# Performance work log

Hardware: AMD Instinct MI355X
Metric: run time of the kernel (lower is better)

## Reference

```python
import jax, jax.numpy as jnp
import numpy as np

B, N, C = 2, 2048, 1024
H, D = 16, 64  # n_q_heads, head_dim
EPS = 1e-6


def setup_inputs() -> dict:
    key = jax.random.key(0)
    ks = jax.random.split(key, 6)
    x = jax.random.normal(ks[0], (B, N, C), dtype=jnp.float32)
    context = jax.random.normal(ks[1], (B, N, C), dtype=jnp.float32)
    # realistic RoPE tables, rotary_dim = head_dim (non-interleaved GLM-style)
    inv_freq = 1.0 / (10000.0 ** (np.arange(0, D, 2, dtype=np.float32) / D))
    ang = np.arange(N, dtype=np.float32)[:, None] * inv_freq[None, :]  # [N, D/2]
    ang = np.concatenate([ang, ang], axis=-1)  # [N, D]
    cos = jnp.broadcast_to(jnp.cos(ang)[None], (B, N, D)).astype(jnp.float32)
    sin = jnp.broadcast_to(jnp.sin(ang)[None], (B, N, D)).astype(jnp.float32)
    s = 1.0 / np.sqrt(C)
    Wq = jax.random.normal(ks[2], (2 * C, C), dtype=jnp.float32) * s
    Wkv = jax.random.normal(ks[3], (2 * C, C), dtype=jnp.float32) * s
    Wo = jax.random.normal(ks[4], (C, C), dtype=jnp.float32) * s
    bo = jnp.zeros((C,), dtype=jnp.float32)
    q_norm_w = jnp.ones((D,), dtype=jnp.float32)
    k_norm_w = jnp.ones((D,), dtype=jnp.float32)
    return {"x": x, "context": context, "cos": cos, "sin": sin,
            "Wq": Wq, "Wkv": Wkv, "Wo": Wo, "bo": bo,
            "q_norm_w": q_norm_w, "k_norm_w": k_norm_w}


def _zm_rmsnorm(t, w):
    # zero-mean RMSNorm over last (head_dim) axis: LayerNorm without bias
    t = t - jnp.mean(t, axis=-1, keepdims=True)
    var = jnp.mean(t * t, axis=-1, keepdims=True)
    return t * jax.lax.rsqrt(var + EPS) * w


def _rotate_half(t):
    t1, t2 = jnp.split(t, 2, axis=-1)
    return jnp.concatenate([-t2, t1], axis=-1)


def reference(x, context, cos, sin, Wq, Wkv, Wo, bo, q_norm_w, k_norm_w):
    b, n1, c = x.shape
    n2 = context.shape[1]
    # fused q+gate projection: [b, n1, 2*C] -> [b, n1, H, 2D], per-head chunk
    qg = (x @ Wq.T).reshape(b, n1, H, 2 * D)
    q = qg[..., :D]                      # [b, n1, H, D]
    gate = qg[..., D:].reshape(b, n1, H * D)  # [b, n1, C]
    q = _zm_rmsnorm(q, q_norm_w).transpose(0, 2, 1, 3)  # [b, H, n1, D]
    # fused k+v projection: [b, n2, 2*C] -> [b, n2, H, 2D]
    kv = (context @ Wkv.T).reshape(b, n2, H, 2 * D)
    k = _zm_rmsnorm(kv[..., :D], k_norm_w).transpose(0, 2, 1, 3)  # [b, H, n2, D]
    v = kv[..., D:].transpose(0, 2, 1, 3)                         # [b, H, n2, D]
    # RoPE (full head_dim rotary)
    cos_b = cos[:, None]  # [b, 1, n, D]
    sin_b = sin[:, None]
    q = q * cos_b + _rotate_half(q) * sin_b
    k = k * cos_b + _rotate_half(k) * sin_b
    # SDPA (non-causal cross attention)
    scale = D ** -0.5
    scores = jnp.einsum('bhqd,bhkd->bhqk', q, k) * scale
    attn = jax.nn.softmax(scores, axis=-1)
    attn_out = jnp.einsum('bhqk,bhkd->bhqd', attn, v)
    attn_out = attn_out.transpose(0, 2, 1, 3).reshape(b, n1, H * D)  # [b, n1, C]
    # gated output combine + out projection
    attn_out = attn_out * jax.nn.sigmoid(gate)
    return attn_out @ Wo.T + bo
```

## Files before the change

kernel.cpp:

```cpp
#include <hip/hip_runtime.h>
#include <cstdint>
#include <cstddef>


#define B_ 2
#define N_ 2048
#define C_ 1024
#define H_ 16
#define D_ 64
#define K_ 1024
#define PK_ 2048
#define EPS_ 1e-6f
#define LOG2E_ 1.44269504088896f
#define SMAX_ 12.0f

typedef __bf16 b16x8 __attribute__((ext_vector_type(8)));
typedef float f32x4 __attribute__((ext_vector_type(4)));

__device__ __forceinline__ unsigned short f2bf(float f) {
  union { float f; unsigned u; } a; a.f = f;
  unsigned r = a.u + 0x7FFFu + ((a.u >> 16) & 1u);
  return (unsigned short)(r >> 16);
}
__device__ __forceinline__ float bf2f(unsigned short u) {
  union { unsigned u; float f; } a; a.u = ((unsigned)u) << 16; return a.f;
}

__device__ __forceinline__ void cast_one(const float* __restrict__ src,
                                         unsigned short* __restrict__ dst, int e) {
  float4 v = *(const float4*)(src + e);
  *(ushort4*)(dst + e) = make_ushort4(f2bf(v.x), f2bf(v.y), f2bf(v.z), f2bf(v.w));
}

__device__ __forceinline__ void pack_one(const float* __restrict__ src,
                                         unsigned short* __restrict__ dst, int e) {
  float4 v = *(const float4*)(src + e);
  const int r = e >> 10, k = e & 1023;
  unsigned short* p = dst + ((size_t)r << 11) + ((k >> 5) << 6) + (k & 31);
  const unsigned short h0 = f2bf(v.x), h1 = f2bf(v.y), h2 = f2bf(v.z), h3 = f2bf(v.w);
  *(ushort4*)p = make_ushort4(h0, h1, h2, h3);
  *(ushort4*)(p + 32) = make_ushort4(f2bf(v.x - bf2f(h0)), f2bf(v.y - bf2f(h1)),
                                     f2bf(v.z - bf2f(h2)), f2bf(v.w - bf2f(h3)));
}

__global__ __launch_bounds__(256) void pack_all(
    const float* __restrict__ x, const float* __restrict__ Wq,
    const float* __restrict__ ctx, const float* __restrict__ Wkv,
    const float* __restrict__ Wo,
    unsigned short* __restrict__ xb, unsigned short* __restrict__ wqb,
    unsigned short* __restrict__ cb, unsigned short* __restrict__ wkvb,
    unsigned short* __restrict__ wop)
{
  const int e = (blockIdx.x * 256 + threadIdx.x) << 2;
  if (e < 4194304)       cast_one(x,   xb,  e);
  else if (e < 6291456)  cast_one(Wq,  wqb, e - 4194304);
  else if (e < 10485760) cast_one(ctx, cb,  e - 6291456);
  else if (e < 12582912) cast_one(Wkv, wkvb, e - 10485760);
  else                   pack_one(Wo,  wop, e - 12582912);
}

__global__ __launch_bounds__(512, 2) void gemm_qkv(
    const unsigned short* __restrict__ xb, const unsigned short* __restrict__ wqb,
    const unsigned short* __restrict__ cb, const unsigned short* __restrict__ wkvb,
    const float* __restrict__ cosb, const float* __restrict__ sinb,
    const float* __restrict__ qnw, const float* __restrict__ knw,
    unsigned short* __restrict__ Qbo, unsigned short* __restrict__ Kbo,
    unsigned short* __restrict__ gate, unsigned short* __restrict__ vt, float qscale)
{
  __shared__ __align__(16) unsigned short As[2][256 * 64];
  __shared__ __align__(16) unsigned short Bs[2][256 * 64];
  const int tid = threadIdx.x, lane = tid & 63, wave = tid >> 6;

  const int id = blockIdx.x;
  const int swz = (id & 7) * 32 + (id >> 3);
  const bool isQ = swz < 128;
  const int local = swz & 127;
  const int bm = (local >> 3) << 8, bn = (local & 7) << 8;
  const int wm = (wave >> 2) << 7, wn = (wave & 3) << 6;

  const unsigned short* Ap = isQ ? xb : cb;
  const unsigned short* Bp = isQ ? wqb : wkvb;

  const int srow = lane >> 3;
  const int sslot = (lane & 7) ^ srow;
  const size_t rbytes = (size_t)K_ * 2;
  const char* aSrc = (const char*)Ap + (size_t)(bm + srow) * rbytes + (sslot << 4);
  const char* bSrc = (const char*)Bp + (size_t)(bn + srow) * rbytes + (sslot << 4);

  f32x4 acc[8][4];
  #pragma unroll
  for (int i = 0; i < 8; ++i)
    #pragma unroll
    for (int j = 0; j < 4; ++j) acc[i][j] = (f32x4){0.f, 0.f, 0.f, 0.f};

  const int fr = lane & 15, fs = lane >> 4;

  #define QSTAGE(buf, kt)                                                          \
    {                                                                              \
      const size_t ko = (size_t)(kt) << 7;                                         \
      _Pragma("unroll")                                                            \
      for (int i = 0; i < 4; ++i) {                                                \
        const int g = (wave << 2) + i;                                             \
        __builtin_amdgcn_global_load_lds(                                          \
            (const __attribute__((address_space(1))) void*)(aSrc + (size_t)(g << 3) * rbytes + ko), \
            (__attribute__((address_space(3))) void*)((char*)As[buf] + (g << 10)), \
            16, 0, 0);                                                             \
        __builtin_amdgcn_global_load_lds(                                          \
            (const __attribute__((address_space(1))) void*)(bSrc + (size_t)(g << 3) * rbytes + ko), \
            (__attribute__((address_space(3))) void*)((char*)Bs[buf] + (g << 10)), \
            16, 0, 0);                                                             \
      }                                                                            \
    }

  QSTAGE(0, 0);
  int cur = 0;
  for (int kt = 0; kt < 16; ++kt) {
    __syncthreads();
    if (kt + 1 < 16) QSTAGE(cur ^ 1, kt + 1);

    const char* Abuf = (const char*)As[cur];
    const char* Bbuf = (const char*)Bs[cur];
    __builtin_amdgcn_s_setprio(1);
    #pragma unroll
    for (int kk = 0; kk < 2; ++kk) {
      b16x8 a[8], b[4];
      #pragma unroll
      for (int mi = 0; mi < 8; ++mi) {
        const int ar = wm + (mi << 4) + fr;
        a[mi] = *(const b16x8*)(Abuf + (ar << 7) + ((((kk << 2) + fs) ^ (ar & 7)) << 4));
      }
      #pragma unroll
      for (int ni = 0; ni < 4; ++ni) {
        const int br = wn + (ni << 4) + fr;
        b[ni] = *(const b16x8*)(Bbuf + (br << 7) + ((((kk << 2) + fs) ^ (br & 7)) << 4));
      }
      #pragma unroll
      for (int mi = 0; mi < 8; ++mi)
        #pragma unroll
        for (int ni = 0; ni < 4; ++ni)
          acc[mi][ni] = __builtin_amdgcn_mfma_f32_16x16x32_bf16(a[mi], b[ni], acc[mi][ni], 0, 0, 0);
    }
    __builtin_amdgcn_s_setprio(0);
    cur ^= 1;
  }
  #undef QSTAGE

  const int g = lane >> 4;
  const int h = (bn >> 7) + (wn >> 7);
  const bool normHalf = ((wn >> 6) & 1) == 0;
  if (normHalf) {
    const float* nw = isQ ? qnw : knw;
    const float oscale = isQ ? qscale : 1.0f;
    unsigned short* nOut = isQ ? Qbo : Kbo;
    float wv[4];
    #pragma unroll
    for (int ni = 0; ni < 4; ++ni) wv[ni] = nw[(ni << 4) + fr];
    #pragma unroll
    for (int mi = 0; mi < 8; ++mi) {
      #pragma unroll
      for (int r = 0; r < 4; ++r) {
        const int t = bm + wm + (mi << 4) + (g << 2) + r;
        float v0 = acc[mi][0][r], v1 = acc[mi][1][r];
        float v2 = acc[mi][2][r], v3 = acc[mi][3][r];
        float s = (v0 + v1) + (v2 + v3);
        #pragma unroll
        for (int off = 1; off < 16; off <<= 1) s += __shfl_xor(s, off);
        const float mean = s * (1.f / 64.f);
        v0 -= mean; v1 -= mean; v2 -= mean; v3 -= mean;
        float s2 = (v0*v0 + v1*v1) + (v2*v2 + v3*v3);
        #pragma unroll
        for (int off = 1; off < 16; off <<= 1) s2 += __shfl_xor(s2, off);
        const float rq = rsqrtf(s2 * (1.f / 64.f) + EPS_);
        const float x0 = v0 * rq * wv[0], x1 = v1 * rq * wv[1];
        const float x2 = v2 * rq * wv[2], x3 = v3 * rq * wv[3];
        const float* cr = cosb + (size_t)t * 64;
        const float* sr = sinb + (size_t)t * 64;
        const float o0 = x0 * cr[fr]    - x2 * sr[fr];
        const float o1 = x1 * cr[16+fr] - x3 * sr[16+fr];
        const float o2 = x2 * cr[32+fr] + x0 * sr[32+fr];
        const float o3 = x3 * cr[48+fr] + x1 * sr[48+fr];
        unsigned short* dp = nOut + (((size_t)((t >> 11) * H_ + h)) * N_ + (t & 2047)) * 64;
        dp[fr]      = f2bf(o0 * oscale);
        dp[16 + fr] = f2bf(o1 * oscale);
        dp[32 + fr] = f2bf(o2 * oscale);
        dp[48 + fr] = f2bf(o3 * oscale);
      }
    }
  } else if (isQ) {
    #pragma unroll
    for (int mi = 0; mi < 8; ++mi)
      #pragma unroll
      for (int r = 0; r < 4; ++r) {
        const int t = bm + wm + (mi << 4) + (g << 2) + r;
        unsigned short* gp = gate + (size_t)t * C_ + h * 64;
        #pragma unroll
        for (int ni = 0; ni < 4; ++ni) gp[(ni << 4) + fr] = f2bf(acc[mi][ni][r]);
      }
  } else {
    #pragma unroll
    for (int mi = 0; mi < 8; ++mi) {
      const int t0 = bm + wm + (mi << 4) + (g << 2);
      const int bb = t0 >> 11, n0 = t0 & 2047;
      #pragma unroll
      for (int ni = 0; ni < 4; ++ni) {
        const int dv = (ni << 4) + fr;
        ushort4 pk = make_ushort4(f2bf(acc[mi][ni][0]), f2bf(acc[mi][ni][1]),
                                  f2bf(acc[mi][ni][2]), f2bf(acc[mi][ni][3]));
        *(ushort4*)(vt + ((size_t)(bb * H_ + h) * 64 + dv) * N_ + n0) = pk;
      }
    }
  }
}

__global__ __launch_bounds__(256) void gemm_nt_hilo(
    const unsigned short* __restrict__ Ap, const unsigned short* __restrict__ Bp,
    float* __restrict__ Cm, int M, int N, const float* __restrict__ bias)
{
  __shared__ __align__(16) unsigned short As[128 * 64];
  __shared__ __align__(16) unsigned short Bs[64 * 64];
  const int tid = threadIdx.x, lane = tid & 63, wave = tid >> 6;

  const int nwg = gridDim.x, id = blockIdx.x;
  const int swz = (id & 7) * (nwg >> 3) + (id >> 3);
  const int nbn = N >> 6;
  const int bm = (swz / nbn) << 7, bn = (swz % nbn) << 6;
  const int wm = (wave >> 1) << 6, wn = (wave & 1) << 5;

  const int srow = lane >> 3;
  const int sslot = (lane & 7) ^ srow;
  const size_t rbytes = (size_t)K_ * 4;
  const char* aSrc = (const char*)Ap + (size_t)(bm + srow) * rbytes + (sslot << 4);
  const char* bSrc = (const char*)Bp + (size_t)(bn + srow) * rbytes + (sslot << 4);

  f32x4 acc[4][2];
  #pragma unroll
  for (int i = 0; i < 4; ++i)
    #pragma unroll
    for (int j = 0; j < 2; ++j) acc[i][j] = (f32x4){0.f, 0.f, 0.f, 0.f};

  const int fr = lane & 15, fs = lane >> 4;
  const int hoff = (fs ^ (fr & 7)) << 4;

  for (int ks = 0; ks < K_ / 32; ++ks) {
    const size_t ko = (size_t)ks << 7;
    #pragma unroll
    for (int i = 0; i < 4; ++i) {
      const int ga = (wave << 2) + i;
      __builtin_amdgcn_global_load_lds(
          (const __attribute__((address_space(1))) void*)(aSrc + (size_t)(ga << 3) * rbytes + ko),
          (__attribute__((address_space(3))) void*)((char*)As + (ga << 10)), 16, 0, 0);
    }
    #pragma unroll
    for (int i = 0; i < 2; ++i) {
      const int gb = (wave << 1) + i;
      __builtin_amdgcn_global_load_lds(
          (const __attribute__((address_space(1))) void*)(bSrc + (size_t)(gb << 3) * rbytes + ko),
          (__attribute__((address_space(3))) void*)((char*)Bs + (gb << 10)), 16, 0, 0);
    }
    __syncthreads();

    b16x8 ah[4], al[4], bh[2], bl[2];
    #pragma unroll
    for (int t = 0; t < 4; ++t) {
      const char* pa = (const char*)As + ((wm + (t << 4) + fr) << 7);
      ah[t] = *(const b16x8*)(pa + hoff);
      al[t] = *(const b16x8*)(pa + (hoff ^ 64));
    }
    #pragma unroll
    for (int t = 0; t < 2; ++t) {
      const char* pb = (const char*)Bs + ((wn + (t << 4) + fr) << 7);
      bh[t] = *(const b16x8*)(pb + hoff);
      bl[t] = *(const b16x8*)(pb + (hoff ^ 64));
    }
    #pragma unroll
    for (int mi = 0; mi < 4; ++mi)
      #pragma unroll
      for (int ni = 0; ni < 2; ++ni) {
        acc[mi][ni] = __builtin_amdgcn_mfma_f32_16x16x32_bf16(ah[mi], bh[ni], acc[mi][ni], 0, 0, 0);
        acc[mi][ni] = __builtin_amdgcn_mfma_f32_16x16x32_bf16(al[mi], bh[ni], acc[mi][ni], 0, 0, 0);
        acc[mi][ni] = __builtin_amdgcn_mfma_f32_16x16x32_bf16(ah[mi], bl[ni], acc[mi][ni], 0, 0, 0);
      }
    __syncthreads();
  }

  const int rbase = (lane >> 4) << 2;
  #pragma unroll
  for (int mi = 0; mi < 4; ++mi)
    #pragma unroll
    for (int ni = 0; ni < 2; ++ni) {
      const int n = bn + wn + (ni << 4) + fr;
      const float badd = bias ? bias[n] : 0.f;
      #pragma unroll
      for (int r = 0; r < 4; ++r) {
        const int m = bm + wm + (mi << 4) + rbase + r;
        Cm[(size_t)m * N + n] = acc[mi][ni][r] + badd;
      }
    }
}

__global__ __launch_bounds__(256) void flash_bf16(
    const unsigned short* __restrict__ Qb, const unsigned short* __restrict__ Kb,
    const unsigned short* __restrict__ Vt, const unsigned short* __restrict__ gateb,
    unsigned short* __restrict__ gp)
{
  const int id = blockIdx.x;
  const int swzb = (id & 7) * 64 + (id >> 3);
  const int q0 = (swzb & 15) * 128;
  const int h = (swzb >> 4) & 15;
  const int b = swzb >> 8;
  const int tid = threadIdx.x, lane = tid & 63, wave = tid >> 6;
  __shared__ __align__(16) unsigned short Ks[2][64 * 64];
  __shared__ __align__(16) unsigned short Vss[2][64 * 64];
  __shared__ __align__(16) __bf16 Ps[4][2][16][72];
  const int bh = b * H_ + h;
  const int g = lane >> 4, fr = lane & 15;

  b16x8 qA0, qA1, qB0, qB1;
  {
    const unsigned short* QrowA = Qb + ((size_t)bh * N_ + q0 + wave*32 + fr) * D_;
    qA0 = *(const b16x8*)(QrowA + (g << 3));
    qA1 = *(const b16x8*)(QrowA + 32 + (g << 3));
    qB0 = *(const b16x8*)(QrowA + 16 * D_ + (g << 3));
    qB1 = *(const b16x8*)(QrowA + 16 * D_ + 32 + (g << 3));
  }

  f32x4 oA[4], oB[4];
  #pragma unroll
  for (int r = 0; r < 4; ++r) {
    oA[r] = (f32x4){0.f, 0.f, 0.f, 0.f};
    oB[r] = (f32x4){0.f, 0.f, 0.f, 0.f};
  }
  float lA = 0.f, lB = 0.f;

  const unsigned short* Kbh  = Kb + (size_t)bh * N_ * D_;
  const unsigned short* Vtbh = Vt + (size_t)bh * D_ * N_;
  const int swzK = ((lane & 7) ^ (lane >> 3)) << 4;
  __bf16* PwA = &Ps[wave][0][0][0] + fr * 72;
  __bf16* PwB = &Ps[wave][1][0][0] + fr * 72;

  #define STAGE(buf, j0)                                                          \
    {                                                                             \
      _Pragma("unroll")                                                           \
      for (int i = 0; i < 2; ++i) {                                               \
        const int gg = wave * 2 + i;                                              \
        const char* ksrc = (const char*)(Kbh + (size_t)((j0) + gg * 8) * D_) +    \
                           (lane >> 3) * 128 + swzK;                              \
        __builtin_amdgcn_global_load_lds(                                         \
            (const __attribute__((address_space(1))) void*)ksrc,                  \
            (__attribute__((address_space(3))) void*)((char*)Ks[buf] + gg * 1024),\
            16, 0, 0);                                                            \
        const int dv = gg * 8 + (lane >> 3);                                      \
        const char* vsrc = (const char*)(Vtbh + (size_t)dv * N_ + (j0)) + swzK;   \
        __builtin_amdgcn_global_load_lds(                                         \
            (const __attribute__((address_space(1))) void*)vsrc,                  \
            (__attribute__((address_space(3))) void*)((char*)Vss[buf] + gg * 1024),\
            16, 0, 0);                                                            \
      }                                                                           \
    }

  STAGE(0, 0);
  int cur = 0;
  for (int j0 = 0; j0 < N_; j0 += 64) {
    __syncthreads();
    if (j0 + 64 < N_) STAGE(cur ^ 1, j0 + 64);

    const unsigned short* Kbuf = Ks[cur];
    const unsigned short* Vbuf = Vss[cur];
    const int cb0 = g << 4;
    __builtin_amdgcn_s_setprio(1);
    #pragma unroll
    for (int t = 0; t < 4; ++t) {
      const int krow = t * 16 + fr;
      const char* kbp = (const char*)Kbuf + krow * 128;
      const int f = (krow & 7) << 4;
      b16x8 kf0 = *(const b16x8*)(kbp + (cb0 ^ f));
      b16x8 kf1 = *(const b16x8*)(kbp + ((64 + cb0) ^ f));
      f32x4 sA = __builtin_amdgcn_mfma_f32_16x16x32_bf16(kf0, qA0, (f32x4){0.f,0.f,0.f,0.f}, 0, 0, 0);
      sA = __builtin_amdgcn_mfma_f32_16x16x32_bf16(kf1, qA1, sA, 0, 0, 0);
      f32x4 sB = __builtin_amdgcn_mfma_f32_16x16x32_bf16(kf0, qB0, (f32x4){0.f,0.f,0.f,0.f}, 0, 0, 0);
      sB = __builtin_amdgcn_mfma_f32_16x16x32_bf16(kf1, qB1, sB, 0, 0, 0);
      union { __bf16 hb[4]; ushort4 u4; } pkA, pkB;
      #pragma unroll
      for (int r = 0; r < 4; ++r) {
        const float pA = __builtin_amdgcn_exp2f(sA[r] - SMAX_);
        lA += pA;
        pkA.hb[r] = (__bf16)pA;
        const float pB = __builtin_amdgcn_exp2f(sB[r] - SMAX_);
        lB += pB;
        pkB.hb[r] = (__bf16)pB;
      }
      *(ushort4*)(PwA + t * 16 + (g << 2)) = pkA.u4;
      *(ushort4*)(PwB + t * 16 + (g << 2)) = pkB.u4;
    }
    __builtin_amdgcn_s_setprio(0);

    b16x8 pfA[2], pfB[2];
    #pragma unroll
    for (int c = 0; c < 2; ++c) {
      pfA[c] = *(const b16x8*)(PwA + c * 32 + (g << 3));
      pfB[c] = *(const b16x8*)(PwB + c * 32 + (g << 3));
    }

    __builtin_amdgcn_s_setprio(1);
    #pragma unroll
    for (int dt = 0; dt < 4; ++dt) {
      const int vrow = dt * 16 + fr;
      const char* vbp = (const char*)Vbuf + vrow * 128;
      const int fv = (vrow & 7) << 4;
      #pragma unroll
      for (int c = 0; c < 2; ++c) {
        b16x8 vf = *(const b16x8*)(vbp + ((c * 64 + cb0) ^ fv));
        oA[dt] = __builtin_amdgcn_mfma_f32_16x16x32_bf16(pfA[c], vf, oA[dt], 0, 0, 0);
        oB[dt] = __builtin_amdgcn_mfma_f32_16x16x32_bf16(pfB[c], vf, oB[dt], 0, 0, 0);
      }
    }
    __builtin_amdgcn_s_setprio(0);
    cur ^= 1;
  }
  #undef STAGE

  lA += __shfl_xor(lA, 16); lA += __shfl_xor(lA, 32);
  lB += __shfl_xor(lB, 16); lB += __shfl_xor(lB, 32);

  #pragma unroll
  for (int r = 0; r < 4; ++r) {
    const float lqA = __shfl(lA, (g << 2) + r);
    const float lqB = __shfl(lB, (g << 2) + r);
    #pragma unroll
    for (int set = 0; set < 2; ++set) {
      const float inv = 1.f / (set ? lqB : lqA);
      const int q = q0 + wave * 32 + set * 16 + (g << 2) + r;
      const size_t qa = (size_t)(b * N_ + q);
      #pragma unroll
      for (int dt = 0; dt < 4; ++dt) {
        const int d = (dt << 4) + fr;
        const float o = (set ? oB[dt][r] : oA[dt][r]) * inv;
        const float gate = bf2f(gateb[qa * C_ + h * 64 + d]);
        const float sg = 1.f / (1.f + __expf(-gate));
        const float val = o * sg;
        const int k = h * 64 + d;
        unsigned short* p = gp + qa * PK_ + ((k >> 5) << 6) + (k & 31);
        const unsigned short hi = f2bf(val);
        p[0]  = hi;
        p[32] = f2bf(val - bf2f(hi));
      }
    }
  }
}

extern "C" void kernel_launch(void* const* d_in, const int* in_sizes, int n_in,
                              void* d_out, int out_size, void* d_ws, size_t ws_size,
                              hipStream_t stream) {
  const float* x    = (const float*)d_in[0];
  const float* ctx  = (const float*)d_in[1];
  const float* cosb = (const float*)d_in[2];
  const float* sinb = (const float*)d_in[3];
  const float* Wq   = (const float*)d_in[4];
  const float* Wkv  = (const float*)d_in[5];
  const float* Wo   = (const float*)d_in[6];
  const float* bo   = (const float*)d_in[7];
  const float* qnw  = (const float*)d_in[8];
  const float* knw  = (const float*)d_in[9];
  float* out = (float*)d_out;

  char* ws = (char*)d_ws;
  unsigned short* Qb   = (unsigned short*)(ws);
  unsigned short* Kb   = (unsigned short*)(ws + (size_t)8388608);
  unsigned short* Vt   = (unsigned short*)(ws + (size_t)16777216);
  unsigned short* gate = (unsigned short*)(ws + (size_t)25165824);
  unsigned short* gpk  = (unsigned short*)(ws + (size_t)41943040);
  unsigned short* xb   = (unsigned short*)(ws + (size_t)58720256);
  unsigned short* cb   = (unsigned short*)(ws + (size_t)67108864);
  unsigned short* wqb  = (unsigned short*)(ws + (size_t)75497472);
  unsigned short* wkvb = (unsigned short*)(ws + (size_t)79691776);
  unsigned short* wop  = (unsigned short*)(ws + (size_t)83886080);

  pack_all<<<dim3(13312), dim3(256), 0, stream>>>(x, Wq, ctx, Wkv, Wo, xb, wqb, cb, wkvb, wop);
  gemm_qkv<<<dim3(256), dim3(512), 0, stream>>>(xb, wqb, cb, wkvb, cosb, sinb, qnw, knw,
                                                Qb, Kb, gate, Vt, 0.125f * LOG2E_);
  flash_bf16<<<dim3(512), dim3(256), 0, stream>>>(Qb, Kb, Vt, gate, gpk);
  gemm_nt_hilo<<<dim3(512), dim3(256), 0, stream>>>(gpk, wop, out, 4096, 1024, bo);
}
```

Before: 150.4 us.

## Load K fragments directly into registers with double-buffered prefetch

The K tile no longer goes through LDS via global_load_lds. Each wave reads its K MFMA fragments straight from global memory into registers, one tile ahead, ping-ponging between two register sets while V keeps its LDS double buffer. This drops the K LDS traffic and its footprint but increases register pressure. Every wave also redundantly loads the same K rows from global/L2 instead of sharing one staged copy.

```diff
diff --git a/kernel.cpp b/kernel.cpp
--- a/kernel.cpp
+++ b/kernel.cpp
@@ -309,7 +309,6 @@
   const int h = (swzb >> 4) & 15;
   const int b = swzb >> 8;
   const int tid = threadIdx.x, lane = tid & 63, wave = tid >> 6;
-  __shared__ __align__(16) unsigned short Ks[2][64 * 64];
   __shared__ __align__(16) unsigned short Vss[2][64 * 64];
   __shared__ __align__(16) __bf16 Ps[4][2][16][72];
   const int bh = b * H_ + h;
@@ -338,17 +337,11 @@
   __bf16* PwA = &Ps[wave][0][0][0] + fr * 72;
   __bf16* PwB = &Ps[wave][1][0][0] + fr * 72;
 
-  #define STAGE(buf, j0)                                                          \
+  #define STAGE_V(buf, j0)                                                        \
     {                                                                             \
       _Pragma("unroll")                                                           \
       for (int i = 0; i < 2; ++i) {                                               \
         const int gg = wave * 2 + i;                                              \
-        const char* ksrc = (const char*)(Kbh + (size_t)((j0) + gg * 8) * D_) +    \
-                           (lane >> 3) * 128 + swzK;                              \
-        __builtin_amdgcn_global_load_lds(                                         \
-            (const __attribute__((address_space(1))) void*)ksrc,                  \
-            (__attribute__((address_space(3))) void*)((char*)Ks[buf] + gg * 1024),\
-            16, 0, 0);                                                            \
         const int dv = gg * 8 + (lane >> 3);                                      \
         const char* vsrc = (const char*)(Vtbh + (size_t)dv * N_ + (j0)) + swzK;   \
         __builtin_amdgcn_global_load_lds(                                         \
@@ -358,66 +351,74 @@
       }                                                                           \
     }
 
-  STAGE(0, 0);
-  int cur = 0;
-  for (int j0 = 0; j0 < N_; j0 += 64) {
-    __syncthreads();
-    if (j0 + 64 < N_) STAGE(cur ^ 1, j0 + 64);
-
-    const unsigned short* Kbuf = Ks[cur];
-    const unsigned short* Vbuf = Vss[cur];
-    const int cb0 = g << 4;
-    __builtin_amdgcn_s_setprio(1);
-    #pragma unroll
-    for (int t = 0; t < 4; ++t) {
-      const int krow = t * 16 + fr;
-      const char* kbp = (const char*)Kbuf + krow * 128;
-      const int f = (krow & 7) << 4;
-      b16x8 kf0 = *(const b16x8*)(kbp + (cb0 ^ f));
-      b16x8 kf1 = *(const b16x8*)(kbp + ((64 + cb0) ^ f));
-      f32x4 sA = __builtin_amdgcn_mfma_f32_16x16x32_bf16(kf0, qA0, (f32x4){0.f,0.f,0.f,0.f}, 0, 0, 0);
-      sA = __builtin_amdgcn_mfma_f32_16x16x32_bf16(kf1, qA1, sA, 0, 0, 0);
-      f32x4 sB = __builtin_amdgcn_mfma_f32_16x16x32_bf16(kf0, qB0, (f32x4){0.f,0.f,0.f,0.f}, 0, 0, 0);
-      sB = __builtin_amdgcn_mfma_f32_16x16x32_bf16(kf1, qB1, sB, 0, 0, 0);
-      union { __bf16 hb[4]; ushort4 u4; } pkA, pkB;
-      #pragma unroll
-      for (int r = 0; r < 4; ++r) {
-        const float pA = __builtin_amdgcn_exp2f(sA[r] - SMAX_);
-        lA += pA;
-        pkA.hb[r] = (__bf16)pA;
-        const float pB = __builtin_amdgcn_exp2f(sB[r] - SMAX_);
-        lB += pB;
-        pkB.hb[r] = (__bf16)pB;
-      }
-      *(ushort4*)(PwA + t * 16 + (g << 2)) = pkA.u4;
-      *(ushort4*)(PwB + t * 16 + (g << 2)) = pkB.u4;
-    }
-    __builtin_amdgcn_s_setprio(0);
-
-    b16x8 pfA[2], pfB[2];
-    #pragma unroll
-    for (int c = 0; c < 2; ++c) {
-      pfA[c] = *(const b16x8*)(PwA + c * 32 + (g << 3));
-      pfB[c] = *(const b16x8*)(PwB + c * 32 + (g << 3));
-    }
-
-    __builtin_amdgcn_s_setprio(1);
-    #pragma unroll
-    for (int dt = 0; dt < 4; ++dt) {
-      const int vrow = dt * 16 + fr;
-      const char* vbp = (const char*)Vbuf + vrow * 128;
-      const int fv = (vrow & 7) << 4;
-      #pragma unroll
-      for (int c = 0; c < 2; ++c) {
-        b16x8 vf = *(const b16x8*)(vbp + ((c * 64 + cb0) ^ fv));
-        oA[dt] = __builtin_amdgcn_mfma_f32_16x16x32_bf16(pfA[c], vf, oA[dt], 0, 0, 0);
-        oB[dt] = __builtin_amdgcn_mfma_f32_16x16x32_bf16(pfB[c], vf, oB[dt], 0, 0, 0);
-      }
-    }
-    __builtin_amdgcn_s_setprio(0);
-    cur ^= 1;
-  }
-  #undef STAGE
+  #define LOADK(K0, K1, j0)                                                       \
+    {                                                                             \
+      _Pragma("unroll")                                                           \
+      for (int t = 0; t < 4; ++t) {                                               \
+        const unsigned short* kr = Kbh + (size_t)((j0) + t * 16 + fr) * D_ + (g << 3); \
+        K0[t] = *(const b16x8*)(kr);                                              \
+        K1[t] = *(const b16x8*)(kr + 32);                                         \
+      }                                                                           \
+    }
+
+  #define TILE(KC0, KC1, KN0, KN1, buf, j0, jn)                                   \
+    {                                                                             \
+      __syncthreads();                             \
+      if ((jn) < N_) { STAGE_V((buf) ^ 1, jn); LOADK(KN0, KN1, jn); }             \
+      const int cb0 = g << 4;                                                     \
+      __builtin_amdgcn_s_setprio(1);                                              \
+      _Pragma("unroll")                                                           \
+      for (int t = 0; t < 4; ++t) {                                               \
+        f32x4 sA = __builtin_amdgcn_mfma_f32_16x16x32_bf16(KC0[t], qA0, (f32x4){0.f,0.f,0.f,0.f}, 0, 0, 0); \
+        sA = __builtin_amdgcn_mfma_f32_16x16x32_bf16(KC1[t], qA1, sA, 0, 0, 0);   \
+        f32x4 sB = __builtin_amdgcn_mfma_f32_16x16x32_bf16(KC0[t], qB0, (f32x4){0.f,0.f,0.f,0.f}, 0, 0, 0); \
+        sB = __builtin_amdgcn_mfma_f32_16x16x32_bf16(KC1[t], qB1, sB, 0, 0, 0);   \
+        union { __bf16 hb[4]; ushort4 u4; } pkA, pkB;                             \
+        _Pragma("unroll")                                                         \
+        for (int r = 0; r < 4; ++r) {                                             \
+          const float pA = __builtin_amdgcn_exp2f(sA[r] - SMAX_);                 \
+          lA += pA;                                                               \
+          pkA.hb[r] = (__bf16)pA;                                                 \
+          const float pB = __builtin_amdgcn_exp2f(sB[r] - SMAX_);                 \
+          lB += pB;                                                               \
+          pkB.hb[r] = (__bf16)pB;                                                 \
+        }                                                                         \
+        *(ushort4*)(PwA + t * 16 + (g << 2)) = pkA.u4;                            \
+        *(ushort4*)(PwB + t * 16 + (g << 2)) = pkB.u4;                            \
+      }                                                                           \
+      __builtin_amdgcn_s_setprio(0);                                              \
+      b16x8 pfA[2], pfB[2];                                                       \
+      _Pragma("unroll")                                                           \
+      for (int c = 0; c < 2; ++c) {                                               \
+        pfA[c] = *(const b16x8*)(PwA + c * 32 + (g << 3));                        \
+        pfB[c] = *(const b16x8*)(PwB + c * 32 + (g << 3));                        \
+      }                                                                           \
+      __builtin_amdgcn_s_setprio(1);                                              \
+      _Pragma("unroll")                                                           \
+      for (int dt = 0; dt < 4; ++dt) {                                            \
+        const int vrow = dt * 16 + fr;                                            \
+        const char* vbp = (const char*)Vss[buf] + vrow * 128;                     \
+        const int fv = (vrow & 7) << 4;                                           \
+        _Pragma("unroll")                                                         \
+        for (int c = 0; c < 2; ++c) {                                             \
+          b16x8 vf = *(const b16x8*)(vbp + ((c * 64 + cb0) ^ fv));                \
+          oA[dt] = __builtin_amdgcn_mfma_f32_16x16x32_bf16(pfA[c], vf, oA[dt], 0, 0, 0); \
+          oB[dt] = __builtin_amdgcn_mfma_f32_16x16x32_bf16(pfB[c], vf, oB[dt], 0, 0, 0); \
+        }                                                                         \
+      }                                                                           \
+      __builtin_amdgcn_s_setprio(0);                                              \
+    }
+
+  b16x8 kX0[4], kX1[4], kY0[4], kY1[4];
+  STAGE_V(0, 0);
+  LOADK(kX0, kX1, 0);
+  for (int jp = 0; jp < N_; jp += 128) {
+    TILE(kX0, kX1, kY0, kY1, 0, jp,      jp + 64);
+    TILE(kY0, kY1, kX0, kX1, 1, jp + 64, jp + 128);
+  }
+  #undef TILE
+  #undef LOADK
+  #undef STAGE_V
 
   lA += __shfl_xor(lA, 16); lA += __shfl_xor(lA, 32);
   lB += __shfl_xor(lB, 16); lB += __shfl_xor(lB, 32);
```

Measured after the change: 163.0 us. 8.4% more time.
